# Performance work log

Measured on AMD Instinct MI355X. Metric: run time of the kernel, lower is better.

Reference implementation:

```python
import jax, jax.numpy as jnp
import numpy as np

DIM = 64          # RefineNet dim
MDIM = 32         # EGNN m_dim
NLAY = 16         # 4 refine stages x n_layer=4 EGNN layers
VOCAB = 26        # len(RNAAlphabet)
PAD = 1           # padding_idx
NPOS = 4096 + PAD + 1
N = 23            # atoms per residue (hard-coded repeat(1,1,23))
EIN = 2 * DIM + 1 # edge MLP input dim

silu = jax.nn.silu

def _lin(x, w, b):
    return x @ w + b

def _egnn(feats, coors, p):
    ew1, eb1, ew2, eb2, cw1, cb1, cw2, cb2, nw1, nb1, nw2, nb2, g, beta = p
    B, Nn, D = feats.shape
    rel = coors[:, :, None, :] - coors[:, None, :, :]            # [B,Nn,Nn,3]
    dist = jnp.sum(rel * rel, -1, keepdims=True)                 # [B,Nn,Nn,1]
    fi = jnp.broadcast_to(feats[:, :, None, :], (B, Nn, Nn, D))
    fj = jnp.broadcast_to(feats[:, None, :, :], (B, Nn, Nn, D))
    edge_in = jnp.concatenate([fi, fj, dist], -1)                # [B,Nn,Nn,2D+1]
    m_ij = silu(_lin(silu(_lin(edge_in, ew1, eb1)), ew2, eb2))   # [B,Nn,Nn,MDIM]
    w = _lin(silu(_lin(m_ij, cw1, cb1)), cw2, cb2)[..., 0]       # [B,Nn,Nn]
    nrm = jnp.sqrt(dist)
    normed = rel / jnp.maximum(nrm, 1e-8)
    # CoorsNorm uses LayerNorm over a size-1 dim: (x - mean) == 0, so phase == beta
    phase = g * jnp.zeros_like(nrm) + beta
    coors_out = jnp.einsum('bij,bijc->bic', w * (1.0 / 50.0), phase * normed) + coors
    m_i = m_ij.sum(-2)
    node_out = _lin(silu(_lin(jnp.concatenate([feats, m_i], -1), nw1, nb1)), nw2, nb2) + feats
    return node_out, coors_out

def _forward(tokens, cords, tok_emb, pos_emb, ew1, eb1, ew2, eb2,
             cw1, cb1, cw2, cb2, nw1, nb1, nw2, nb2, ln_g, ln_b):
    stacked = (ew1, eb1, ew2, eb2, cw1, cb1, cw2, cb2, nw1, nb1, nw2, nb2, ln_g, ln_b)
    t = tokens[:, 0, :]                                  # [b,l]
    b, l = t.shape
    tok = jnp.broadcast_to(t[:, :, None], (b, l, N))     # repeat(1,1,23)
    fea = tok_emb[tok]                                   # [b,l,N,DIM]
    mask = (tok.reshape(b * l, N) != PAD).astype(jnp.int32)
    pos = jnp.cumsum(mask, axis=1) * mask + PAD
    fea = fea + pos_emb[pos].reshape(fea.shape)
    co = cords.reshape(b, l, N, 3)

    def run(f, c, start):
        for k in range(4):
            p = tuple(a[start + k] for a in stacked)
            f, c = _egnn(f, c, p)
        return f, c

    f, c = run(fea.reshape(b * l, N, DIM), co.reshape(b * l, N, 3), 0)
    f = jnp.swapaxes(f.reshape(b, l, N, DIM), 1, 2)
    c = jnp.swapaxes(c.reshape(b, l, N, 3), 1, 2)
    f, c = run(f.reshape(b * N, l, DIM), c.reshape(b * N, l, 3), 4)
    f = jnp.swapaxes(f.reshape(b, N, l, DIM), 1, 2)
    c = jnp.swapaxes(c.reshape(b, N, l, 3), 1, 2)
    f, c = run(f.reshape(b * l, N, DIM), c.reshape(b * l, N, 3), 8)
    f = jnp.swapaxes(f.reshape(b, l, N, DIM), 1, 2)
    c = jnp.swapaxes(c.reshape(b, l, N, 3), 1, 2)
    f, c = run(f.reshape(b * N, l, DIM), c.reshape(b * N, l, 3), 12)
    c = jnp.swapaxes(c.reshape(b, N, l, 3), 1, 2)
    return c.reshape(b, l * N, 3)

def setup_inputs():
    key = jax.random.key(0)
    ks = jax.random.split(key, 20)
    b, l = 2, 96
    s = 0.02
    def W(k, shp):
        return jax.random.normal(k, shp, jnp.float32) * s
    return {
        "tokens": jax.random.randint(ks[0], (b, 1, l), 0, VOCAB),
        "cords": jax.random.normal(ks[1], (b, l * N, 3), jnp.float32),
        "tok_emb": W(ks[2], (VOCAB, DIM)),
        "pos_emb": W(ks[3], (NPOS, DIM)).at[PAD].set(0.0),
        "ew1": W(ks[4], (NLAY, EIN, EIN * 2)), "eb1": W(ks[5], (NLAY, EIN * 2)),
        "ew2": W(ks[6], (NLAY, EIN * 2, MDIM)), "eb2": W(ks[7], (NLAY, MDIM)),
        "cw1": W(ks[8], (NLAY, MDIM, MDIM * 4)), "cb1": W(ks[9], (NLAY, MDIM * 4)),
        "cw2": W(ks[10], (NLAY, MDIM * 4, 1)), "cb2": W(ks[11], (NLAY, 1)),
        "nw1": W(ks[12], (NLAY, DIM + MDIM, DIM * 2)), "nb1": W(ks[13], (NLAY, DIM * 2)),
        "nw2": W(ks[14], (NLAY, DIM * 2, DIM)), "nb2": W(ks[15], (NLAY, DIM)),
        "ln_g": 1.0 + W(ks[16], (NLAY, 1)),
        "ln_b": W(ks[17], (NLAY, 1)),
    }

def reference(tokens, cords, tok_emb, pos_emb, ew1, eb1, ew2, eb2,
              cw1, cb1, cw2, cb2, nw1, nb1, nw2, nb2, ln_g, ln_b):
    return _forward(tokens, cords, tok_emb, pos_emb, ew1, eb1, ew2, eb2,
                    cw1, cb1, cw2, cb2, nw1, nb1, nw2, nb2, ln_g, ln_b)
```

## Files before the change

### kernel.cpp

```cpp
#include <hip/hip_runtime.h>
#include <math.h>

#define DIM   64
#define MDIM  32
#define NLAY  16
#define PAD   1
#define NB    2
#define LL    96
#define NN    23
#define NNODE (NB*LL*NN)
#define EIN   129
#define EH    258
#define KP    272
#define NK0   17
#define NH    128
#define BPITCH 276
#define APITCH 276
#define NOUT  516
#define NTILE 17
#define XP    104
#define HP    136
#define OP    560

typedef __attribute__((ext_vector_type(8)))  short        bf16x8;
typedef __attribute__((ext_vector_type(16))) float        f32x16;
typedef __attribute__((ext_vector_type(4)))  unsigned int uint4v;
typedef __attribute__((ext_vector_type(2)))  float        f32x2;
typedef __attribute__((ext_vector_type(4)))  float        f32x4;

__device__ __forceinline__ f32x2 mk2(float a, float b) { f32x2 r; r.x = a; r.y = b; return r; }

__device__ __forceinline__ float silu_f(float x) {
    float e = __expf(-x);
    return x * __builtin_amdgcn_rcpf(1.0f + e);
}
__device__ __forceinline__ f32x2 silu2(f32x2 x) {
    f32x2 t = x * (-1.44269504f);
    f32x2 e;
    e.x = __builtin_amdgcn_exp2f(t.x);
    e.y = __builtin_amdgcn_exp2f(t.y);
    f32x2 den = e + 1.0f;
    f32x2 r;
    r.x = __builtin_amdgcn_rcpf(den.x);
    r.y = __builtin_amdgcn_rcpf(den.y);
    return x * r;
}
__device__ __forceinline__ unsigned short bf16_rn(float x) {
    unsigned u = __float_as_uint(x);
    u += 0x7FFF + ((u >> 16) & 1);
    return (unsigned short)(u >> 16);
}
__device__ __forceinline__ float bf16_up(unsigned short h) {
    return __uint_as_float(((unsigned)h) << 16);
}
__device__ __forceinline__ f32x2 ub2(unsigned bw) {
    return mk2(__uint_as_float(bw << 16), __uint_as_float(bw & 0xFFFF0000u));
}
__device__ __forceinline__ unsigned hpack(f32x2 a2, f32x2 w2, f32x2 b2, f32x2 d2) {
    f32x2 x2 = a2 + b2;
    x2 = __builtin_elementwise_fma(d2, w2, x2);
    f32x2 h2 = silu2(x2);
    return __builtin_amdgcn_perm(__float_as_uint(h2.y), __float_as_uint(h2.x), 0x07060302u);
}
__device__ __forceinline__ int fwd_map(int nf, int alongL) {
    if (alongL) {
        int b = nf / (LL * NN);
        int rem = nf % (LL * NN);
        int l = rem / NN, n = rem % NN;
        return (b * NN + n) * LL + l;
    }
    return nf;
}
__device__ __forceinline__ int inv_map(int gnode, int alongL) {
    if (alongL) {
        int g = gnode / LL, l = gnode % LL;
        int b = g / NN, n = g % NN;
        return (b * LL + l) * NN + n;
    }
    return gnode;
}

__global__ void k_embed(const int* __restrict__ tokens,
                        const float* __restrict__ tok_emb,
                        const float* __restrict__ pos_emb,
                        float* __restrict__ feats) {
    int idx = blockIdx.x * blockDim.x + threadIdx.x;
    if (idx < NNODE * DIM) {
        int node = idx / DIM, d = idx % DIM;
        int b = node / (LL * NN);
        int rem = node % (LL * NN);
        int n = rem % NN;
        int l = rem / NN;
        int t = tokens[b * LL + l];
        float f = tok_emb[t * DIM + d];
        if (t != PAD) f += pos_emb[(n + 2) * DIM + d];
        feats[idx] = f;
    }
}

__global__ void k_prep(const float* __restrict__ ew1, const float* __restrict__ ew2,
                       const float* __restrict__ cw1, const float* __restrict__ cb1,
                       const float* __restrict__ cw2,
                       const float* __restrict__ nw1, const float* __restrict__ nw2,
                       float* __restrict__ wdF, unsigned short* __restrict__ ew2P,
                       unsigned short* __restrict__ cw1P,
                       float* __restrict__ cbwP,
                       unsigned short* __restrict__ ew1P,
                       unsigned short* __restrict__ nw1P,
                       unsigned short* __restrict__ nw2P) {
    int idx = blockIdx.x * blockDim.x + threadIdx.x;
    if (idx < NLAY * KP) {
        int L = idx / KP, k = idx % KP;
        float v = (k < EH) ? ew1[(size_t)L * EIN * EH + 128 * EH + k] : 0.0f;
        wdF[idx] = bf16_up(bf16_rn(v));
    }
    if (idx < NLAY * NK0 * 512) {
        int L = idx / (NK0 * 512); int r = idx % (NK0 * 512);
        int k0 = r / 512; int r2 = r % 512;
        int lane = r2 >> 3, j = r2 & 7;
        int k = k0 * 16 + (lane >> 5) * 8 + j;
        int n = lane & 31;
        float v = (k < EH) ? ew2[((size_t)L * EH + k) * MDIM + n] : 0.0f;
        ew2P[idx] = bf16_rn(v);
    }
    if (idx < NLAY * 4096) {
        int L = idx / 4096; int r = idx % 4096;
        int mb = r / 1024; int r2 = r % 1024;
        int k0 = r2 / 512; int r3 = r2 % 512;
        int lane = r3 >> 3, j = r3 & 7;
        int k = k0 * 16 + (lane >> 5) * 8 + j;
        int o = mb * 32 + (lane & 31);
        cw1P[idx] = bf16_rn(cw1[((size_t)L * MDIM + k) * NH + o]);
    }
    if (idx < NLAY * 128) {
        int L = idx / 128; int r = idx % 128;
        int hlf = r / 64; int r2 = r % 64;
        int mb = r2 / 16, reg = r2 % 16;
        int o = mb * 32 + (reg & 3) + 8 * (reg >> 2) + 4 * hlf;
        cbwP[(size_t)L * 256 + r * 2 + 0] = cb1[L * NH + o];
        cbwP[(size_t)L * 256 + r * 2 + 1] = cw2[L * NH + o];
    }
    if (idx < NLAY * NTILE * 4 * 512) {
        int L = idx / (NTILE * 4 * 512); int r = idx % (NTILE * 4 * 512);
        int nt = r / 2048; int r2 = r % 2048;
        int ks = r2 / 512; int r3 = r2 % 512;
        int lane = r3 >> 3, j = r3 & 7;
        int d = ks * 16 + (lane >> 5) * 8 + j;
        int o = nt * 32 + (lane & 31);
        float v = 0.0f;
        if (o < EH)        v = ew1[(size_t)L * EIN * EH + d * EH + o];
        else if (o < NOUT) v = ew1[(size_t)L * EIN * EH + (DIM + d) * EH + (o - EH)];
        ew1P[idx] = bf16_rn(v);
    }
    if (idx < NLAY * 4 * 6 * 512) {
        int L = idx / 12288; int r = idx % 12288;
        int nt = r / 3072; int r2 = r % 3072;
        int ks = r2 / 512; int r3 = r2 % 512;
        int lane = r3 >> 3, j = r3 & 7;
        int k = ks * 16 + (lane >> 5) * 8 + j;
        int n = nt * 32 + (lane & 31);
        nw1P[idx] = bf16_rn(nw1[((size_t)L * (DIM + MDIM) + k) * NH + n]);
    }
    if (idx < NLAY * 2 * 8 * 512) {
        int L = idx / 8192; int r = idx % 8192;
        int nt = r / 4096; int r2 = r % 4096;
        int ks = r2 / 512; int r3 = r2 % 512;
        int lane = r3 >> 3, j = r3 & 7;
        int k = ks * 16 + (lane >> 5) * 8 + j;
        int n = nt * 32 + (lane & 31);
        nw2P[idx] = bf16_rn(nw2[((size_t)L * NH + k) * DIM + n]);
    }
}

__global__ __launch_bounds__(256)
void k_np(const float* __restrict__ fIn, const float* __restrict__ coSrc,
          const float* __restrict__ miL, const float* __restrict__ dL,
          const unsigned short* __restrict__ nw1PL, const float* __restrict__ nb1L,
          const unsigned short* __restrict__ nw2PL, const float* __restrict__ nb2L,
          const unsigned short* __restrict__ ew1PL, const float* __restrict__ eb1L,
          float* __restrict__ fOut, float* __restrict__ coDst,
          float* __restrict__ miNext, float* __restrict__ dNext,
          unsigned short* __restrict__ aH, unsigned short* __restrict__ bH,
          int aL0, int aL1, int doNode) {
    __shared__ unsigned short xS[32 * XP];
    __shared__ unsigned short hS[32 * HP];
    __shared__ unsigned short outS[32 * OP];
    __shared__ int gsrcS[32], gdstS[32];

    int n0  = blockIdx.x * 32;
    int tid = threadIdx.x;
    int wave = tid >> 6, lane = tid & 63, half = lane >> 5, e = lane & 31;

    if (tid < 32) {
        gsrcS[tid] = fwd_map(n0 + tid, aL0);
        gdstS[tid] = fwd_map(n0 + tid, aL1);
    }
    __syncthreads();

    for (int i = 0; i < 8; i++) {
        int x = tid + 256 * i;
        int node = x >> 6, d = x & 63;
        xS[node * XP + d] = bf16_rn(fIn[(n0 + node) * DIM + d]);
    }
    if (doNode) {
        for (int i = 0; i < 4; i++) {
            int x = tid + 256 * i;
            int node = x >> 5, d = x & 31;
            xS[node * XP + DIM + d] = bf16_rn(miL[(size_t)gsrcS[node] * MDIM + d]);
        }
    }
    for (int x = tid; x < 32 * 14; x += 256) {
        int node = x / 14, c = EH + x % 14;
        outS[node * OP + c] = 0;
    }
    if (tid < 96) {
        int node = tid / 3, c = tid % 3;
        int gs = gsrcS[node], gd = gdstS[node];
        float cv = coSrc[gs * 3 + c] + (doNode ? dL[gs * 3 + c] : 0.0f);
        coDst[gd * 3 + c] = cv;
        dNext[gd * 3 + c] = 0.0f;
    }
    for (int i = 0; i < 4; i++) {
        int x = tid + 256 * i;
        int node = x >> 5, d = x & 31;
        miNext[(size_t)gdstS[node] * MDIM + d] = 0.0f;
    }
    __syncthreads();

    if (doNode) {
        {
            int nt = wave;
            f32x16 acc;
#pragma unroll
            for (int q = 0; q < 16; q++) acc[q] = 0.0f;
#pragma unroll
            for (int ks = 0; ks < 6; ks++) {
                uint4v au = *(const uint4v*)(xS + e * XP + ks * 16 + half * 8);
                uint4v bu = *(const uint4v*)(nw1PL + ((size_t)(nt * 6 + ks) * 512 + lane * 8));
                acc = __builtin_amdgcn_mfma_f32_32x32x16_bf16(
                          __builtin_bit_cast(bf16x8, au),
                          __builtin_bit_cast(bf16x8, bu), acc, 0, 0, 0);
            }
            int o = nt * 32 + e;
            float b1 = nb1L[o];
#pragma unroll
            for (int q = 0; q < 16; q++) {
                int row = (q & 3) + 8 * (q >> 2) + 4 * half;
                hS[row * HP + o] = bf16_rn(silu_f(acc[q] + b1));
            }
        }
        __syncthreads();

        if (wave < 2) {
            int nt = wave;
            f32x16 acc;
#pragma unroll
            for (int q = 0; q < 16; q++) acc[q] = 0.0f;
#pragma unroll
            for (int ks = 0; ks < 8; ks++) {
                uint4v au = *(const uint4v*)(hS + e * HP + ks * 16 + half * 8);
                uint4v bu = *(const uint4v*)(nw2PL + ((size_t)(nt * 8 + ks) * 512 + lane * 8));
                acc = __builtin_amdgcn_mfma_f32_32x32x16_bf16(
                          __builtin_bit_cast(bf16x8, au),
                          __builtin_bit_cast(bf16x8, bu), acc, 0, 0, 0);
            }
            int o = nt * 32 + e;
            float b2 = nb2L[o];
#pragma unroll
            for (int q = 0; q < 16; q++) {
                int row = (q & 3) + 8 * (q >> 2) + 4 * half;
                float fo = acc[q] + b2 + bf16_up(xS[row * XP + o]);
                fOut[(size_t)(n0 + row) * DIM + o] = fo;
                xS[row * XP + o] = bf16_rn(fo);
            }
        }
        __syncthreads();
    }

    {
        uint4v afrag[4];
#pragma unroll
        for (int ks = 0; ks < 4; ks++)
            afrag[ks] = *(const uint4v*)(xS + e * XP + ks * 16 + half * 8);

        for (int nt = wave; nt < NTILE; nt += 4) {
            f32x16 acc;
#pragma unroll
            for (int q = 0; q < 16; q++) acc[q] = 0.0f;
#pragma unroll
            for (int ks = 0; ks < 4; ks++) {
                uint4v bu = *(const uint4v*)(ew1PL + ((size_t)(nt * 4 + ks) * 512 + lane * 8));
                acc = __builtin_amdgcn_mfma_f32_32x32x16_bf16(
                          __builtin_bit_cast(bf16x8, afrag[ks]),
                          __builtin_bit_cast(bf16x8, bu), acc, 0, 0, 0);
            }
            int o = nt * 32 + e;
            float eb = (o < EH) ? eb1L[o] : 0.0f;
            int col = (o < EH) ? o : (o + 14);
#pragma unroll
            for (int q = 0; q < 16; q++) {
                int row = (q & 3) + 8 * (q >> 2) + 4 * half;
                float v = (o < NOUT) ? (acc[q] + eb) : 0.0f;
                outS[row * OP + col] = bf16_rn(v);
            }
        }
    }
    __syncthreads();

    for (int x = tid; x < 32 * 68; x += 256) {
        int row = x / 68, off = x % 68;
        int gd = gdstS[row];
        uint4v v = *(const uint4v*)(outS + row * OP + off * 8);
        if (off < 34) *(uint4v*)(aH + (size_t)gd * KP + off * 8) = v;
        else          *(uint4v*)(bH + (size_t)gd * KP + (off - 34) * 8) = v;
    }
}

__global__ __launch_bounds__(256, 3)
void k_edge(const unsigned short* __restrict__ aH,
            const unsigned short* __restrict__ bH,
            const float* __restrict__ coorsO,
            const float* __restrict__ wdFL,
            const unsigned short* __restrict__ ew2PL,
            const float* __restrict__ eb2L,
            const unsigned short* __restrict__ cw1PL,
            const float* __restrict__ cbwPL,
            const float* __restrict__ cb2L,
            const float* __restrict__ lnbL,
            float* __restrict__ miBuf, float* __restrict__ deltaBuf,
            int Nn, int itpg, int njt) {
    __shared__ unsigned short bS[32 * BPITCH];
    __shared__ __align__(16) float aSf[8 * APITCH];
    __shared__ __align__(16) float wdS[KP];
    __shared__ float cjS[32 * 3];
    __shared__ __align__(16) float cbwS[256];
    __shared__ unsigned short mT[4][32 * 36];

    int bid = blockIdx.x;
    int g   = bid / (itpg * njt);
    int r   = bid % (itpg * njt);
    int it  = r / njt;
    int jt  = r % njt;

    int tid  = threadIdx.x;
    int wave = tid >> 6, lane = tid & 63, half = lane >> 5, e = lane & 31;

    int j0  = jt * 32;
    int njr = Nn - j0; if (njr > 32) njr = 32;
    int i0  = it * 8;
    int nir = Nn - i0; if (nir > 8) nir = 8;

    {
        const unsigned int* src = (const unsigned int*)(bH + (size_t)(g * Nn + j0) * KP);
        unsigned int* dst = (unsigned int*)bS;
        int tot = njr * 136;
        for (int x = tid; x < tot; x += 256) {
            int rr = x / 136, c = x % 136;
            dst[rr * (BPITCH / 2) + c] = src[rr * 136 + c];
        }
        const unsigned short* asrc = aH + (size_t)(g * Nn + i0) * KP;
        int at = nir * KP;
        for (int x = tid; x < at; x += 256) {
            int rr = x / KP, k = x % KP;
            aSf[rr * APITCH + k] = bf16_up(asrc[rr * KP + k]);
        }
        for (int x = tid; x < KP; x += 256) wdS[x] = wdFL[x];
        if (tid < njr * 3) cjS[tid] = coorsO[(g * Nn + j0) * 3 + tid];
        if (tid < 256) cbwS[tid] = cbwPL[tid];
    }
    __syncthreads();

    float eb2v = eb2L[e];
    float beta = lnbL[0];
    float cb2v = cb2L[0];

    int  jc     = (e < njr) ? e : (njr - 1);
    bool jvalid = (e < njr);
    float cjx = cjS[jc * 3 + 0], cjy = cjS[jc * 3 + 1], cjz = cjS[jc * 3 + 2];

    unsigned short* mW = &mT[wave][0];
    const unsigned short* bRow = bS + jc * BPITCH;

    int il0 = wave * 2, il1 = wave * 2 + 1;
    bool v0 = il0 < nir, v1 = il1 < nir;
    int gi0 = g * Nn + i0 + (v0 ? il0 : 0);
    int gi1 = g * Nn + i0 + (v1 ? il1 : 0);

    float rx0, ry0, rz0, d0, rx1, ry1, rz1, d1;
    {
        float cx = coorsO[gi0 * 3 + 0], cy = coorsO[gi0 * 3 + 1], cz = coorsO[gi0 * 3 + 2];
        rx0 = cx - cjx; ry0 = cy - cjy; rz0 = cz - cjz;
        d0 = rx0 * rx0 + ry0 * ry0 + rz0 * rz0;
        cx = coorsO[gi1 * 3 + 0]; cy = coorsO[gi1 * 3 + 1]; cz = coorsO[gi1 * 3 + 2];
        rx1 = cx - cjx; ry1 = cy - cjy; rz1 = cz - cjz;
        d1 = rx1 * rx1 + ry1 * ry1 + rz1 * rz1;
    }
    f32x2 d20 = mk2(d0, d0), d21 = mk2(d1, d1);
    const float* aR0 = aSf + (v0 ? il0 : 0) * APITCH;
    const float* aR1 = aSf + (v1 ? il1 : 0) * APITCH;

    f32x16 acc0, acc1;
#pragma unroll
    for (int q = 0; q < 16; q++) { acc0[q] = 0.0f; acc1[q] = 0.0f; }

#pragma unroll
    for (int k0 = 0; k0 < NK0; k0++) {
        int ko = k0 * 16 + half * 8;
        uint2 bA = *(const uint2*)(bRow + ko);
        uint2 bB = *(const uint2*)(bRow + ko + 4);
        f32x4 wv0 = *(const f32x4*)(wdS + ko);
        f32x4 wv1 = *(const f32x4*)(wdS + ko + 4);
        uint4v eu = *(const uint4v*)(ew2PL + ((size_t)k0 * 64 + lane) * 8);
        f32x2 b2_0 = ub2(bA.x), b2_1 = ub2(bA.y), b2_2 = ub2(bB.x), b2_3 = ub2(bB.y);

        f32x4 a00 = *(const f32x4*)(aR0 + ko);
        f32x4 a01 = *(const f32x4*)(aR0 + ko + 4);
        uint4v hu0;
        hu0[0] = hpack(a00.xy, wv0.xy, b2_0, d20);
        hu0[1] = hpack(a00.zw, wv0.zw, b2_1, d20);
        hu0[2] = hpack(a01.xy, wv1.xy, b2_2, d20);
        hu0[3] = hpack(a01.zw, wv1.zw, b2_3, d20);
        acc0 = __builtin_amdgcn_mfma_f32_32x32x16_bf16(
                   __builtin_bit_cast(bf16x8, hu0),
                   __builtin_bit_cast(bf16x8, eu), acc0, 0, 0, 0);

        f32x4 a10 = *(const f32x4*)(aR1 + ko);
        f32x4 a11 = *(const f32x4*)(aR1 + ko + 4);
        uint4v hu1;
        hu1[0] = hpack(a10.xy, wv0.xy, b2_0, d21);
        hu1[1] = hpack(a10.zw, wv0.zw, b2_1, d21);
        hu1[2] = hpack(a11.xy, wv1.xy, b2_2, d21);
        hu1[3] = hpack(a11.zw, wv1.zw, b2_3, d21);
        acc1 = __builtin_amdgcn_mfma_f32_32x32x16_bf16(
                   __builtin_bit_cast(bf16x8, hu1),
                   __builtin_bit_cast(bf16x8, eu), acc1, 0, 0, 0);
    }

    f32x2 ebp = mk2(eb2v, eb2v);

#pragma unroll
    for (int s = 0; s < 2; s++) {
        if (!(s ? v1 : v0)) continue;
        int gi = s ? gi1 : gi0;
        float rx = s ? rx1 : rx0, ry = s ? ry1 : ry0, rz = s ? rz1 : rz0;
        float dist = s ? d1 : d0;

        float mv[16];
        f32x2 mi2 = mk2(0.0f, 0.0f);
        if (njr == 32) {
#pragma unroll
            for (int qp = 0; qp < 8; qp++) {
                int q = qp * 2;
                f32x2 x2 = mk2(s ? acc1[q] : acc0[q], s ? acc1[q + 1] : acc0[q + 1]) + ebp;
                f32x2 m2 = silu2(x2);
                mv[q] = m2.x; mv[q + 1] = m2.y;
                mi2 += m2;
            }
        } else {
#pragma unroll
            for (int qp = 0; qp < 8; qp++) {
                int q = qp * 2;
                f32x2 x2 = mk2(s ? acc1[q] : acc0[q], s ? acc1[q + 1] : acc0[q + 1]) + ebp;
                f32x2 m2 = silu2(x2);
                int row0 = (q & 3) + 8 * (q >> 2) + 4 * half;
                if (j0 + row0 >= Nn) m2.x = 0.0f;
                if (j0 + row0 + 1 >= Nn) m2.y = 0.0f;
                mv[q] = m2.x; mv[q + 1] = m2.y;
                mi2 += m2;
            }
        }
        float miAcc = mi2.x + mi2.y;

#pragma unroll
        for (int q = 0; q < 4; q++) {
            unsigned lo = __builtin_amdgcn_perm(__float_as_uint(mv[q * 4 + 1]),
                                                __float_as_uint(mv[q * 4 + 0]), 0x07060302u);
            unsigned hi = __builtin_amdgcn_perm(__float_as_uint(mv[q * 4 + 3]),
                                                __float_as_uint(mv[q * 4 + 2]), 0x07060302u);
            int row0 = 8 * q + 4 * half;
            *(uint2*)&mW[e * 36 + row0] = make_uint2(lo, hi);
        }

        miAcc += __shfl_xor(miAcc, 32, 64);
        if (half == 0) atomicAdd(&miBuf[gi * MDIM + e], miAcc);

        bf16x8 bq[2];
#pragma unroll
        for (int k0 = 0; k0 < 2; k0++) {
            uint4v t;
#pragma unroll
            for (int p = 0; p < 4; p++) {
                unsigned w0 = mW[(k0 * 16 + half * 8 + 2 * p    ) * 36 + e];
                unsigned w1 = mW[(k0 * 16 + half * 8 + 2 * p + 1) * 36 + e];
                t[p] = w0 | (w1 << 16);
            }
            bq[k0] = __builtin_bit_cast(bf16x8, t);
        }

        f32x2 w2a = mk2(0.0f, 0.0f);
#pragma unroll
        for (int mb = 0; mb < 4; mb++) {
            f32x16 sacc;
#pragma unroll
            for (int q = 0; q < 16; q++) sacc[q] = 0.0f;
#pragma unroll
            for (int k0 = 0; k0 < 2; k0++) {
                uint4v cu = *(const uint4v*)(cw1PL + ((size_t)(mb * 2 + k0) * 64 + lane) * 8);
                sacc = __builtin_amdgcn_mfma_f32_32x32x16_bf16(
                           __builtin_bit_cast(bf16x8, cu), bq[k0], sacc, 0, 0, 0);
            }
            const f32x4* cv = (const f32x4*)(cbwS + (half * 4 + mb) * 32);
#pragma unroll
            for (int qp = 0; qp < 8; qp++) {
                f32x4 c4 = cv[qp];
                f32x2 s2 = mk2(sacc[2 * qp], sacc[2 * qp + 1]) + mk2(c4.x, c4.z);
                f32x2 p2 = silu2(s2);
                w2a = __builtin_elementwise_fma(p2, mk2(c4.y, c4.w), w2a);
            }
        }
        float wAcc = w2a.x + w2a.y;
        wAcc += __shfl_xor(wAcc, 32, 64);
        float w = wAcc + cb2v;
        float nrm = sqrtf(dist);
        float scale = (w * 0.02f) * beta * __builtin_amdgcn_rcpf(fmaxf(nrm, 1e-8f));

        float dAx = 0.0f, dAy = 0.0f, dAz = 0.0f;
        if (jvalid && half == 0) {
            dAx = scale * rx; dAy = scale * ry; dAz = scale * rz;
        }
#pragma unroll
        for (int m = 16; m >= 1; m >>= 1) {
            dAx += __shfl_xor(dAx, m, 64);
            dAy += __shfl_xor(dAy, m, 64);
            dAz += __shfl_xor(dAz, m, 64);
        }
        if (lane == 0) {
            atomicAdd(&deltaBuf[gi * 3 + 0], dAx);
            atomicAdd(&deltaBuf[gi * 3 + 1], dAy);
            atomicAdd(&deltaBuf[gi * 3 + 2], dAz);
        }
    }
}

__global__ void k_fin(const float* __restrict__ co, const float* __restrict__ dl,
                      float* __restrict__ out) {
    int idx = blockIdx.x * blockDim.x + threadIdx.x;
    if (idx < NNODE * 3) {
        int gnode = idx / 3, c = idx % 3;
        int nf = inv_map(gnode, 1);
        out[nf * 3 + c] = co[idx] + dl[idx];
    }
}

extern "C" void kernel_launch(void* const* d_in, const int* in_sizes, int n_in,
                              void* d_out, int out_size, void* d_ws, size_t ws_size,
                              hipStream_t stream) {
    (void)in_sizes; (void)n_in; (void)out_size; (void)ws_size;

    const int*   tokens  = (const int*)d_in[0];
    const float* cords   = (const float*)d_in[1];
    const float* tok_emb = (const float*)d_in[2];
    const float* pos_emb = (const float*)d_in[3];
    const float* ew1 = (const float*)d_in[4];
    const float* eb1 = (const float*)d_in[5];
    const float* ew2 = (const float*)d_in[6];
    const float* eb2 = (const float*)d_in[7];
    const float* cw1 = (const float*)d_in[8];
    const float* cb1 = (const float*)d_in[9];
    const float* cw2 = (const float*)d_in[10];
    const float* cb2 = (const float*)d_in[11];
    const float* nw1 = (const float*)d_in[12];
    const float* nb1 = (const float*)d_in[13];
    const float* nw2 = (const float*)d_in[14];
    const float* nb2 = (const float*)d_in[15];
    const float* lnb = (const float*)d_in[17];

    float* wf = (float*)d_ws;
    float* featsA = wf; wf += NNODE * DIM;
    float* featsB = wf; wf += NNODE * DIM;
    float* coorsO0 = wf; wf += NNODE * 3;
    float* coorsO1 = wf; wf += NNODE * 3;
    float* mi0  = wf; wf += NNODE * MDIM;
    float* mi1  = wf; wf += NNODE * MDIM;
    float* dl0  = wf; wf += NNODE * 3;
    float* dl1  = wf; wf += NNODE * 3;
    float* cbwP = wf; wf += NLAY * 256;
    float* wdF  = wf; wf += NLAY * KP;

    uintptr_t p = (uintptr_t)wf; p = (p + 15) & ~(uintptr_t)15;
    unsigned short* wh = (unsigned short*)p;
    unsigned short* aHb  = wh; wh += (size_t)NNODE * KP;
    unsigned short* bHb  = wh; wh += (size_t)NNODE * KP;
    unsigned short* ew2P = wh; wh += NLAY * NK0 * 512;
    unsigned short* cw1P = wh; wh += NLAY * 4096;
    unsigned short* ew1P = wh; wh += (size_t)NLAY * NTILE * 4 * 512;
    unsigned short* nw1P = wh; wh += (size_t)NLAY * 4 * 6 * 512;
    unsigned short* nw2P = wh; wh += (size_t)NLAY * 2 * 8 * 512;

    float* coorsO[2] = {coorsO0, coorsO1};
    float* miB[2]    = {mi0, mi1};
    float* dlB[2]    = {dl0, dl1};

    int prepN = NLAY * NTILE * 4 * 512;
    k_prep<<<(prepN + 255) / 256, 256, 0, stream>>>(
        ew1, ew2, cw1, cb1, cw2, nw1, nw2,
        wdF, ew2P, cw1P, cbwP, ew1P, nw1P, nw2P);
    k_embed<<<(NNODE * DIM + 255) / 256, 256, 0, stream>>>(
        tokens, tok_emb, pos_emb, featsA);

    float* fCur = featsA; float* fNxt = featsB;

    k_np<<<NNODE / 32, 256, 0, stream>>>(
        fCur, cords, nullptr, nullptr,
        nullptr, nullptr, nullptr, nullptr,
        ew1P + 0, eb1 + 0,
        fNxt, coorsO[0], miB[0], dlB[0],
        aHb, bHb, 0, 0, 0);

    for (int L = 0; L < NLAY; L++) {
        int alongL = (L / 4) % 2;
        int idx  = L & 1;
        int Nn   = alongL ? LL : NN;
        int njt  = alongL ? 3 : 1;
        int itpg = (Nn + 7) / 8;
        int groups = NNODE / Nn;

        k_edge<<<groups * itpg * njt, 256, 0, stream>>>(
            aHb, bHb, coorsO[idx],
            wdF + L * KP, ew2P + (size_t)L * NK0 * 512, eb2 + L * MDIM,
            cw1P + (size_t)L * 4096, cbwP + (size_t)L * 256,
            cb2 + L, lnb + L, miB[idx], dlB[idx], Nn, itpg, njt);

        if (L < NLAY - 1) {
            int aL1 = ((L + 1) / 4) % 2;
            int nidx = (L + 1) & 1;
            k_np<<<NNODE / 32, 256, 0, stream>>>(
                fCur, coorsO[idx], miB[idx], dlB[idx],
                nw1P + (size_t)L * 4 * 6 * 512, nb1 + L * NH,
                nw2P + (size_t)L * 2 * 8 * 512, nb2 + L * DIM,
                ew1P + (size_t)(L + 1) * NTILE * 4 * 512, eb1 + (size_t)(L + 1) * EH,
                fNxt, coorsO[nidx], miB[nidx], dlB[nidx],
                aHb, bHb, alongL, aL1, 1);
            float* t = fCur; fCur = fNxt; fNxt = t;
        } else {
            k_fin<<<(NNODE * 3 + 255) / 256, 256, 0, stream>>>(
                coorsO[idx], dlB[idx], (float*)d_out);
        }
    }
}
```

Before: 972.0 us.

## Split node-projection kernel across four blocks per tile and batch silu reciprocals

The node/projection kernel now launches four blocks per 32-node tile. Each block computes the node MLP redundantly but only a quarter of the edge-input projection column tiles, with column padding realigned to 18 tiles so each half maps cleanly onto the aH/bH buffers. Separately, silu is evaluated four lanes at a time, sharing one reciprocal across four denominators, in the edge hidden activation, message activation and coordinate-weight MLP. This trades redundant node-MLP work and extra blocks for more parallelism, and trades fewer rcp instructions for extra multiplies and some overflow risk in the product of denominators.

```diff
diff --git a/kernel.cpp b/kernel.cpp
--- a/kernel.cpp
+++ b/kernel.cpp
@@ -16,11 +16,10 @@
 #define NH    128
 #define BPITCH 276
 #define APITCH 276
-#define NOUT  516
-#define NTILE 17
+#define NT2   18
 #define XP    104
 #define HP    136
-#define OP    560
+#define OPS   168
 
 typedef __attribute__((ext_vector_type(8)))  short        bf16x8;
 typedef __attribute__((ext_vector_type(16))) float        f32x16;
@@ -29,21 +28,29 @@
 typedef __attribute__((ext_vector_type(4)))  float        f32x4;
 
 __device__ __forceinline__ f32x2 mk2(float a, float b) { f32x2 r; r.x = a; r.y = b; return r; }
+__device__ __forceinline__ f32x4 mk4(float a, float b, float c, float d) {
+    f32x4 r; r.x = a; r.y = b; r.z = c; r.w = d; return r;
+}
 
 __device__ __forceinline__ float silu_f(float x) {
     float e = __expf(-x);
     return x * __builtin_amdgcn_rcpf(1.0f + e);
 }
-__device__ __forceinline__ f32x2 silu2(f32x2 x) {
-    f32x2 t = x * (-1.44269504f);
-    f32x2 e;
+__device__ __forceinline__ f32x4 silu4(f32x4 x) {
+    f32x4 t = x * (-1.44269504f);
+    f32x4 e;
     e.x = __builtin_amdgcn_exp2f(t.x);
     e.y = __builtin_amdgcn_exp2f(t.y);
-    f32x2 den = e + 1.0f;
-    f32x2 r;
-    r.x = __builtin_amdgcn_rcpf(den.x);
-    r.y = __builtin_amdgcn_rcpf(den.y);
-    return x * r;
+    e.z = __builtin_amdgcn_exp2f(t.z);
+    e.w = __builtin_amdgcn_exp2f(t.w);
+    f32x4 d = e + 1.0f;
+    float p01 = d.x * d.y, p23 = d.z * d.w;
+    float R = __builtin_amdgcn_rcpf(p01 * p23);
+    float R01 = R * p23, R23 = R * p01;
+    f32x4 sg;
+    sg.x = d.y * R01; sg.y = d.x * R01;
+    sg.z = d.w * R23; sg.w = d.z * R23;
+    return x * sg;
 }
 __device__ __forceinline__ unsigned short bf16_rn(float x) {
     unsigned u = __float_as_uint(x);
@@ -53,14 +60,21 @@
 __device__ __forceinline__ float bf16_up(unsigned short h) {
     return __uint_as_float(((unsigned)h) << 16);
 }
-__device__ __forceinline__ f32x2 ub2(unsigned bw) {
-    return mk2(__uint_as_float(bw << 16), __uint_as_float(bw & 0xFFFF0000u));
-}
-__device__ __forceinline__ unsigned hpack(f32x2 a2, f32x2 w2, f32x2 b2, f32x2 d2) {
-    f32x2 x2 = a2 + b2;
-    x2 = __builtin_elementwise_fma(d2, w2, x2);
-    f32x2 h2 = silu2(x2);
-    return __builtin_amdgcn_perm(__float_as_uint(h2.y), __float_as_uint(h2.x), 0x07060302u);
+__device__ __forceinline__ uint2 hpack4(f32x4 a4, f32x4 w4, unsigned bu0, unsigned bu1,
+                                        float dist) {
+    f32x4 b4;
+    b4.x = __uint_as_float(bu0 << 16);
+    b4.y = __uint_as_float(bu0 & 0xFFFF0000u);
+    b4.z = __uint_as_float(bu1 << 16);
+    b4.w = __uint_as_float(bu1 & 0xFFFF0000u);
+    f32x4 x4 = a4 + b4;
+    f32x4 d4 = mk4(dist, dist, dist, dist);
+    x4 = __builtin_elementwise_fma(d4, w4, x4);
+    f32x4 h4 = silu4(x4);
+    uint2 o;
+    o.x = __builtin_amdgcn_perm(__float_as_uint(h4.y), __float_as_uint(h4.x), 0x07060302u);
+    o.y = __builtin_amdgcn_perm(__float_as_uint(h4.w), __float_as_uint(h4.z), 0x07060302u);
+    return o;
 }
 __device__ __forceinline__ int fwd_map(int nf, int alongL) {
     if (alongL) {
@@ -140,16 +154,16 @@
         cbwP[(size_t)L * 256 + r * 2 + 0] = cb1[L * NH + o];
         cbwP[(size_t)L * 256 + r * 2 + 1] = cw2[L * NH + o];
     }
-    if (idx < NLAY * NTILE * 4 * 512) {
-        int L = idx / (NTILE * 4 * 512); int r = idx % (NTILE * 4 * 512);
+    if (idx < NLAY * NT2 * 4 * 512) {
+        int L = idx / (NT2 * 4 * 512); int r = idx % (NT2 * 4 * 512);
         int nt = r / 2048; int r2 = r % 2048;
         int ks = r2 / 512; int r3 = r2 % 512;
         int lane = r3 >> 3, j = r3 & 7;
         int d = ks * 16 + (lane >> 5) * 8 + j;
-        int o = nt * 32 + (lane & 31);
+        int c = nt * 32 + (lane & 31);
         float v = 0.0f;
-        if (o < EH)        v = ew1[(size_t)L * EIN * EH + d * EH + o];
-        else if (o < NOUT) v = ew1[(size_t)L * EIN * EH + (DIM + d) * EH + (o - EH)];
+        if (c < 288) { if (c < EH) v = ew1[(size_t)L * EIN * EH + d * EH + c]; }
+        else { int ob = c - 288; if (ob < EH) v = ew1[(size_t)L * EIN * EH + (DIM + d) * EH + ob]; }
         ew1P[idx] = bf16_rn(v);
     }
     if (idx < NLAY * 4 * 6 * 512) {
@@ -184,10 +198,12 @@
           int aL0, int aL1, int doNode) {
     __shared__ unsigned short xS[32 * XP];
     __shared__ unsigned short hS[32 * HP];
-    __shared__ unsigned short outS[32 * OP];
+    __shared__ unsigned short outS[32 * OPS];
     __shared__ int gsrcS[32], gdstS[32];
 
-    int n0  = blockIdx.x * 32;
+    int bid  = blockIdx.x;
+    int tileB = bid >> 2, par = bid & 3;
+    int n0  = tileB * 32;
     int tid = threadIdx.x;
     int wave = tid >> 6, lane = tid & 63, half = lane >> 5, e = lane & 31;
 
@@ -209,21 +225,19 @@
             xS[node * XP + DIM + d] = bf16_rn(miL[(size_t)gsrcS[node] * MDIM + d]);
         }
     }
-    for (int x = tid; x < 32 * 14; x += 256) {
-        int node = x / 14, c = EH + x % 14;
-        outS[node * OP + c] = 0;
-    }
-    if (tid < 96) {
-        int node = tid / 3, c = tid % 3;
-        int gs = gsrcS[node], gd = gdstS[node];
-        float cv = coSrc[gs * 3 + c] + (doNode ? dL[gs * 3 + c] : 0.0f);
-        coDst[gd * 3 + c] = cv;
-        dNext[gd * 3 + c] = 0.0f;
-    }
-    for (int i = 0; i < 4; i++) {
-        int x = tid + 256 * i;
-        int node = x >> 5, d = x & 31;
-        miNext[(size_t)gdstS[node] * MDIM + d] = 0.0f;
+    if (par == 0) {
+        if (tid < 96) {
+            int node = tid / 3, c = tid % 3;
+            int gs = gsrcS[node], gd = gdstS[node];
+            float cv = coSrc[gs * 3 + c] + (doNode ? dL[gs * 3 + c] : 0.0f);
+            coDst[gd * 3 + c] = cv;
+            dNext[gd * 3 + c] = 0.0f;
+        }
+        for (int i = 0; i < 4; i++) {
+            int x = tid + 256 * i;
+            int node = x >> 5, d = x & 31;
+            miNext[(size_t)gdstS[node] * MDIM + d] = 0.0f;
+        }
     }
     __syncthreads();
 
@@ -270,7 +284,7 @@
             for (int q = 0; q < 16; q++) {
                 int row = (q & 3) + 8 * (q >> 2) + 4 * half;
                 float fo = acc[q] + b2 + bf16_up(xS[row * XP + o]);
-                fOut[(size_t)(n0 + row) * DIM + o] = fo;
+                if (par == 0) fOut[(size_t)(n0 + row) * DIM + o] = fo;
                 xS[row * XP + o] = bf16_rn(fo);
             }
         }
@@ -283,7 +297,9 @@
         for (int ks = 0; ks < 4; ks++)
             afrag[ks] = *(const uint4v*)(xS + e * XP + ks * 16 + half * 8);
 
-        for (int nt = wave; nt < NTILE; nt += 4) {
+        for (int lt = wave; lt < 5; lt += 4) {
+            int nt = par + lt * 4;
+            if (nt >= NT2) continue;
             f32x16 acc;
 #pragma unroll
             for (int q = 0; q < 16; q++) acc[q] = 0.0f;
@@ -294,25 +310,37 @@
                           __builtin_bit_cast(bf16x8, afrag[ks]),
                           __builtin_bit_cast(bf16x8, bu), acc, 0, 0, 0);
             }
-            int o = nt * 32 + e;
-            float eb = (o < EH) ? eb1L[o] : 0.0f;
-            int col = (o < EH) ? o : (o + 14);
+            int c = nt * 32 + e;
+            bool isA = c < 288;
+            int oc = isA ? c : (c - 288);
+            bool valid = oc < EH;
+            float eb = (isA && valid) ? eb1L[oc] : 0.0f;
 #pragma unroll
             for (int q = 0; q < 16; q++) {
                 int row = (q & 3) + 8 * (q >> 2) + 4 * half;
-                float v = (o < NOUT) ? (acc[q] + eb) : 0.0f;
-                outS[row * OP + col] = bf16_rn(v);
+                float v = valid ? (acc[q] + eb) : 0.0f;
+                outS[row * OPS + lt * 32 + e] = bf16_rn(v);
             }
         }
     }
     __syncthreads();
 
-    for (int x = tid; x < 32 * 68; x += 256) {
-        int row = x / 68, off = x % 68;
-        int gd = gdstS[row];
-        uint4v v = *(const uint4v*)(outS + row * OP + off * 8);
-        if (off < 34) *(uint4v*)(aH + (size_t)gd * KP + off * 8) = v;
-        else          *(uint4v*)(bH + (size_t)gd * KP + (off - 34) * 8) = v;
+    {
+        int nch = (par < 2) ? 20 : 16;
+        for (int x = tid; x < 32 * nch; x += 256) {
+            int row = x / nch, cl = x % nch;
+            int lt = cl >> 2, sub = cl & 3;
+            int nt = par + lt * 4;
+            uint4v v = *(const uint4v*)(outS + row * OPS + lt * 32 + sub * 8);
+            int gd = gdstS[row];
+            if (nt < 9) {
+                int col = nt * 32 + sub * 8;
+                if (col < KP) *(uint4v*)(aH + (size_t)gd * KP + col) = v;
+            } else {
+                int col = (nt - 9) * 32 + sub * 8;
+                if (col < KP) *(uint4v*)(bH + (size_t)gd * KP + col) = v;
+            }
+        }
     }
 }
 
@@ -395,7 +423,6 @@
         rx1 = cx - cjx; ry1 = cy - cjy; rz1 = cz - cjz;
         d1 = rx1 * rx1 + ry1 * ry1 + rz1 * rz1;
     }
-    f32x2 d20 = mk2(d0, d0), d21 = mk2(d1, d1);
     const float* aR0 = aSf + (v0 ? il0 : 0) * APITCH;
     const float* aR1 = aSf + (v1 ? il1 : 0) * APITCH;
 
@@ -411,32 +438,27 @@
         f32x4 wv0 = *(const f32x4*)(wdS + ko);
         f32x4 wv1 = *(const f32x4*)(wdS + ko + 4);
         uint4v eu = *(const uint4v*)(ew2PL + ((size_t)k0 * 64 + lane) * 8);
-        f32x2 b2_0 = ub2(bA.x), b2_1 = ub2(bA.y), b2_2 = ub2(bB.x), b2_3 = ub2(bB.y);
 
         f32x4 a00 = *(const f32x4*)(aR0 + ko);
         f32x4 a01 = *(const f32x4*)(aR0 + ko + 4);
+        uint2 h00 = hpack4(a00, wv0, bA.x, bA.y, d0);
+        uint2 h01 = hpack4(a01, wv1, bB.x, bB.y, d0);
         uint4v hu0;
-        hu0[0] = hpack(a00.xy, wv0.xy, b2_0, d20);
-        hu0[1] = hpack(a00.zw, wv0.zw, b2_1, d20);
-        hu0[2] = hpack(a01.xy, wv1.xy, b2_2, d20);
-        hu0[3] = hpack(a01.zw, wv1.zw, b2_3, d20);
+        hu0[0] = h00.x; hu0[1] = h00.y; hu0[2] = h01.x; hu0[3] = h01.y;
         acc0 = __builtin_amdgcn_mfma_f32_32x32x16_bf16(
                    __builtin_bit_cast(bf16x8, hu0),
                    __builtin_bit_cast(bf16x8, eu), acc0, 0, 0, 0);
 
         f32x4 a10 = *(const f32x4*)(aR1 + ko);
         f32x4 a11 = *(const f32x4*)(aR1 + ko + 4);
+        uint2 h10 = hpack4(a10, wv0, bA.x, bA.y, d1);
+        uint2 h11 = hpack4(a11, wv1, bB.x, bB.y, d1);
         uint4v hu1;
-        hu1[0] = hpack(a10.xy, wv0.xy, b2_0, d21);
-        hu1[1] = hpack(a10.zw, wv0.zw, b2_1, d21);
-        hu1[2] = hpack(a11.xy, wv1.xy, b2_2, d21);
-        hu1[3] = hpack(a11.zw, wv1.zw, b2_3, d21);
+        hu1[0] = h10.x; hu1[1] = h10.y; hu1[2] = h11.x; hu1[3] = h11.y;
         acc1 = __builtin_amdgcn_mfma_f32_32x32x16_bf16(
                    __builtin_bit_cast(bf16x8, hu1),
                    __builtin_bit_cast(bf16x8, eu), acc1, 0, 0, 0);
     }
-
-    f32x2 ebp = mk2(eb2v, eb2v);
 
 #pragma unroll
     for (int s = 0; s < 2; s++) {
@@ -446,30 +468,25 @@
         float dist = s ? d1 : d0;
 
         float mv[16];
-        f32x2 mi2 = mk2(0.0f, 0.0f);
-        if (njr == 32) {
-#pragma unroll
-            for (int qp = 0; qp < 8; qp++) {
-                int q = qp * 2;
-                f32x2 x2 = mk2(s ? acc1[q] : acc0[q], s ? acc1[q + 1] : acc0[q + 1]) + ebp;
-                f32x2 m2 = silu2(x2);
-                mv[q] = m2.x; mv[q + 1] = m2.y;
-                mi2 += m2;
-            }
-        } else {
-#pragma unroll
-            for (int qp = 0; qp < 8; qp++) {
-                int q = qp * 2;
-                f32x2 x2 = mk2(s ? acc1[q] : acc0[q], s ? acc1[q + 1] : acc0[q + 1]) + ebp;
-                f32x2 m2 = silu2(x2);
-                int row0 = (q & 3) + 8 * (q >> 2) + 4 * half;
-                if (j0 + row0 >= Nn) m2.x = 0.0f;
-                if (j0 + row0 + 1 >= Nn) m2.y = 0.0f;
-                mv[q] = m2.x; mv[q + 1] = m2.y;
-                mi2 += m2;
-            }
-        }
-        float miAcc = mi2.x + mi2.y;
+        f32x4 mi4 = mk4(0.0f, 0.0f, 0.0f, 0.0f);
+#pragma unroll
+        for (int qg = 0; qg < 4; qg++) {
+            int q = qg * 4;
+            f32x4 x4 = mk4(s ? acc1[q] : acc0[q], s ? acc1[q + 1] : acc0[q + 1],
+                           s ? acc1[q + 2] : acc0[q + 2], s ? acc1[q + 3] : acc0[q + 3])
+                       + eb2v;
+            f32x4 m4 = silu4(x4);
+            if (njr != 32) {
+                int row0 = 8 * qg + 4 * half;
+                if (j0 + row0 + 0 >= Nn) m4.x = 0.0f;
+                if (j0 + row0 + 1 >= Nn) m4.y = 0.0f;
+                if (j0 + row0 + 2 >= Nn) m4.z = 0.0f;
+                if (j0 + row0 + 3 >= Nn) m4.w = 0.0f;
+            }
+            mv[q] = m4.x; mv[q + 1] = m4.y; mv[q + 2] = m4.z; mv[q + 3] = m4.w;
+            mi4 += m4;
+        }
+        float miAcc = (mi4.x + mi4.y) + (mi4.z + mi4.w);
 
 #pragma unroll
         for (int q = 0; q < 4; q++) {
@@ -497,7 +514,7 @@
             bq[k0] = __builtin_bit_cast(bf16x8, t);
         }
 
-        f32x2 w2a = mk2(0.0f, 0.0f);
+        f32x4 w4a = mk4(0.0f, 0.0f, 0.0f, 0.0f);
 #pragma unroll
         for (int mb = 0; mb < 4; mb++) {
             f32x16 sacc;
@@ -511,14 +528,15 @@
             }
             const f32x4* cv = (const f32x4*)(cbwS + (half * 4 + mb) * 32);
 #pragma unroll
-            for (int qp = 0; qp < 8; qp++) {
-                f32x4 c4 = cv[qp];
-                f32x2 s2 = mk2(sacc[2 * qp], sacc[2 * qp + 1]) + mk2(c4.x, c4.z);
-                f32x2 p2 = silu2(s2);
-                w2a = __builtin_elementwise_fma(p2, mk2(c4.y, c4.w), w2a);
-            }
-        }
-        float wAcc = w2a.x + w2a.y;
+            for (int i = 0; i < 4; i++) {
+                f32x4 c0 = cv[2 * i], c1 = cv[2 * i + 1];
+                f32x4 x4 = mk4(sacc[4 * i] + c0.x, sacc[4 * i + 1] + c0.z,
+                               sacc[4 * i + 2] + c1.x, sacc[4 * i + 3] + c1.z);
+                f32x4 p4 = silu4(x4);
+                w4a = __builtin_elementwise_fma(p4, mk4(c0.y, c0.w, c1.y, c1.w), w4a);
+            }
+        }
+        float wAcc = (w4a.x + w4a.y) + (w4a.z + w4a.w);
         wAcc += __shfl_xor(wAcc, 32, 64);
         float w = wAcc + cb2v;
         float nrm = sqrtf(dist);
@@ -593,7 +611,7 @@
     unsigned short* bHb  = wh; wh += (size_t)NNODE * KP;
     unsigned short* ew2P = wh; wh += NLAY * NK0 * 512;
     unsigned short* cw1P = wh; wh += NLAY * 4096;
-    unsigned short* ew1P = wh; wh += (size_t)NLAY * NTILE * 4 * 512;
+    unsigned short* ew1P = wh; wh += (size_t)NLAY * NT2 * 4 * 512;
     unsigned short* nw1P = wh; wh += (size_t)NLAY * 4 * 6 * 512;
     unsigned short* nw2P = wh; wh += (size_t)NLAY * 2 * 8 * 512;
 
@@ -601,7 +619,7 @@
     float* miB[2]    = {mi0, mi1};
     float* dlB[2]    = {dl0, dl1};
 
-    int prepN = NLAY * NTILE * 4 * 512;
+    int prepN = NLAY * NT2 * 4 * 512;
     k_prep<<<(prepN + 255) / 256, 256, 0, stream>>>(
         ew1, ew2, cw1, cb1, cw2, nw1, nw2,
         wdF, ew2P, cw1P, cbwP, ew1P, nw1P, nw2P);
@@ -610,7 +628,7 @@
 
     float* fCur = featsA; float* fNxt = featsB;
 
-    k_np<<<NNODE / 32, 256, 0, stream>>>(
+    k_np<<<(NNODE / 32) * 4, 256, 0, stream>>>(
         fCur, cords, nullptr, nullptr,
         nullptr, nullptr, nullptr, nullptr,
         ew1P + 0, eb1 + 0,
@@ -634,11 +652,11 @@
         if (L < NLAY - 1) {
             int aL1 = ((L + 1) / 4) % 2;
             int nidx = (L + 1) & 1;
-            k_np<<<NNODE / 32, 256, 0, stream>>>(
+            k_np<<<(NNODE / 32) * 4, 256, 0, stream>>>(
                 fCur, coorsO[idx], miB[idx], dlB[idx],
                 nw1P + (size_t)L * 4 * 6 * 512, nb1 + L * NH,
                 nw2P + (size_t)L * 2 * 8 * 512, nb2 + L * DIM,
-                ew1P + (size_t)(L + 1) * NTILE * 4 * 512, eb1 + (size_t)(L + 1) * EH,
+                ew1P + (size_t)(L + 1) * NT2 * 4 * 512, eb1 + (size_t)(L + 1) * EH,
                 fNxt, coorsO[nidx], miB[nidx], dlB[nidx],
                 aHb, bHb, alongL, aL1, 1);
             float* t = fCur; fCur = fNxt; fNxt = t;
```

Result: no change. 962.4 us (-1.0%).

## Split node-projection kernel across four blocks per node tile

Applied to the files above, without the earlier changes.

The k_np kernel now launches four blocks per 32-node tile. Each block recomputes the node MLP redundantly and then produces only a quarter of the edge-projection output tiles, using a column layout repacked to 18 tiles so the A and B halves are padded separately. The goal is more parallelism and better GPU occupancy in a kernel that previously ran few blocks, each doing serial MFMA tile loops. The cost is four times the node-MLP compute and the feature and weight loads, with only block 0 writing the shared outputs.

```diff
diff --git a/kernel.cpp b/kernel.cpp
--- a/kernel.cpp
+++ b/kernel.cpp
@@ -16,11 +16,10 @@
 #define NH    128
 #define BPITCH 276
 #define APITCH 276
-#define NOUT  516
-#define NTILE 17
+#define NT2   18
 #define XP    104
 #define HP    136
-#define OP    560
+#define OPS   168
 
 typedef __attribute__((ext_vector_type(8)))  short        bf16x8;
 typedef __attribute__((ext_vector_type(16))) float        f32x16;
@@ -140,16 +139,16 @@
         cbwP[(size_t)L * 256 + r * 2 + 0] = cb1[L * NH + o];
         cbwP[(size_t)L * 256 + r * 2 + 1] = cw2[L * NH + o];
     }
-    if (idx < NLAY * NTILE * 4 * 512) {
-        int L = idx / (NTILE * 4 * 512); int r = idx % (NTILE * 4 * 512);
+    if (idx < NLAY * NT2 * 4 * 512) {
+        int L = idx / (NT2 * 4 * 512); int r = idx % (NT2 * 4 * 512);
         int nt = r / 2048; int r2 = r % 2048;
         int ks = r2 / 512; int r3 = r2 % 512;
         int lane = r3 >> 3, j = r3 & 7;
         int d = ks * 16 + (lane >> 5) * 8 + j;
-        int o = nt * 32 + (lane & 31);
+        int c = nt * 32 + (lane & 31);
         float v = 0.0f;
-        if (o < EH)        v = ew1[(size_t)L * EIN * EH + d * EH + o];
-        else if (o < NOUT) v = ew1[(size_t)L * EIN * EH + (DIM + d) * EH + (o - EH)];
+        if (c < 288) { if (c < EH) v = ew1[(size_t)L * EIN * EH + d * EH + c]; }
+        else { int ob = c - 288; if (ob < EH) v = ew1[(size_t)L * EIN * EH + (DIM + d) * EH + ob]; }
         ew1P[idx] = bf16_rn(v);
     }
     if (idx < NLAY * 4 * 6 * 512) {
@@ -184,10 +183,12 @@
           int aL0, int aL1, int doNode) {
     __shared__ unsigned short xS[32 * XP];
     __shared__ unsigned short hS[32 * HP];
-    __shared__ unsigned short outS[32 * OP];
+    __shared__ unsigned short outS[32 * OPS];
     __shared__ int gsrcS[32], gdstS[32];
 
-    int n0  = blockIdx.x * 32;
+    int bid  = blockIdx.x;
+    int tileB = bid >> 2, par = bid & 3;
+    int n0  = tileB * 32;
     int tid = threadIdx.x;
     int wave = tid >> 6, lane = tid & 63, half = lane >> 5, e = lane & 31;
 
@@ -209,21 +210,19 @@
             xS[node * XP + DIM + d] = bf16_rn(miL[(size_t)gsrcS[node] * MDIM + d]);
         }
     }
-    for (int x = tid; x < 32 * 14; x += 256) {
-        int node = x / 14, c = EH + x % 14;
-        outS[node * OP + c] = 0;
-    }
-    if (tid < 96) {
-        int node = tid / 3, c = tid % 3;
-        int gs = gsrcS[node], gd = gdstS[node];
-        float cv = coSrc[gs * 3 + c] + (doNode ? dL[gs * 3 + c] : 0.0f);
-        coDst[gd * 3 + c] = cv;
-        dNext[gd * 3 + c] = 0.0f;
-    }
-    for (int i = 0; i < 4; i++) {
-        int x = tid + 256 * i;
-        int node = x >> 5, d = x & 31;
-        miNext[(size_t)gdstS[node] * MDIM + d] = 0.0f;
+    if (par == 0) {
+        if (tid < 96) {
+            int node = tid / 3, c = tid % 3;
+            int gs = gsrcS[node], gd = gdstS[node];
+            float cv = coSrc[gs * 3 + c] + (doNode ? dL[gs * 3 + c] : 0.0f);
+            coDst[gd * 3 + c] = cv;
+            dNext[gd * 3 + c] = 0.0f;
+        }
+        for (int i = 0; i < 4; i++) {
+            int x = tid + 256 * i;
+            int node = x >> 5, d = x & 31;
+            miNext[(size_t)gdstS[node] * MDIM + d] = 0.0f;
+        }
     }
     __syncthreads();
 
@@ -270,7 +269,7 @@
             for (int q = 0; q < 16; q++) {
                 int row = (q & 3) + 8 * (q >> 2) + 4 * half;
                 float fo = acc[q] + b2 + bf16_up(xS[row * XP + o]);
-                fOut[(size_t)(n0 + row) * DIM + o] = fo;
+                if (par == 0) fOut[(size_t)(n0 + row) * DIM + o] = fo;
                 xS[row * XP + o] = bf16_rn(fo);
             }
         }
@@ -283,7 +282,9 @@
         for (int ks = 0; ks < 4; ks++)
             afrag[ks] = *(const uint4v*)(xS + e * XP + ks * 16 + half * 8);
 
-        for (int nt = wave; nt < NTILE; nt += 4) {
+        for (int lt = wave; lt < 5; lt += 4) {
+            int nt = par + lt * 4;
+            if (nt >= NT2) continue;
             f32x16 acc;
 #pragma unroll
             for (int q = 0; q < 16; q++) acc[q] = 0.0f;
@@ -294,25 +295,37 @@
                           __builtin_bit_cast(bf16x8, afrag[ks]),
                           __builtin_bit_cast(bf16x8, bu), acc, 0, 0, 0);
             }
-            int o = nt * 32 + e;
-            float eb = (o < EH) ? eb1L[o] : 0.0f;
-            int col = (o < EH) ? o : (o + 14);
+            int c = nt * 32 + e;
+            bool isA = c < 288;
+            int oc = isA ? c : (c - 288);
+            bool valid = oc < EH;
+            float eb = (isA && valid) ? eb1L[oc] : 0.0f;
 #pragma unroll
             for (int q = 0; q < 16; q++) {
                 int row = (q & 3) + 8 * (q >> 2) + 4 * half;
-                float v = (o < NOUT) ? (acc[q] + eb) : 0.0f;
-                outS[row * OP + col] = bf16_rn(v);
+                float v = valid ? (acc[q] + eb) : 0.0f;
+                outS[row * OPS + lt * 32 + e] = bf16_rn(v);
             }
         }
     }
     __syncthreads();
 
-    for (int x = tid; x < 32 * 68; x += 256) {
-        int row = x / 68, off = x % 68;
-        int gd = gdstS[row];
-        uint4v v = *(const uint4v*)(outS + row * OP + off * 8);
-        if (off < 34) *(uint4v*)(aH + (size_t)gd * KP + off * 8) = v;
-        else          *(uint4v*)(bH + (size_t)gd * KP + (off - 34) * 8) = v;
+    {
+        int nch = (par < 2) ? 20 : 16;
+        for (int x = tid; x < 32 * nch; x += 256) {
+            int row = x / nch, cl = x % nch;
+            int lt = cl >> 2, sub = cl & 3;
+            int nt = par + lt * 4;
+            uint4v v = *(const uint4v*)(outS + row * OPS + lt * 32 + sub * 8);
+            int gd = gdstS[row];
+            if (nt < 9) {
+                int col = nt * 32 + sub * 8;
+                if (col < KP) *(uint4v*)(aH + (size_t)gd * KP + col) = v;
+            } else {
+                int col = (nt - 9) * 32 + sub * 8;
+                if (col < KP) *(uint4v*)(bH + (size_t)gd * KP + col) = v;
+            }
+        }
     }
 }
 
@@ -593,7 +606,7 @@
     unsigned short* bHb  = wh; wh += (size_t)NNODE * KP;
     unsigned short* ew2P = wh; wh += NLAY * NK0 * 512;
     unsigned short* cw1P = wh; wh += NLAY * 4096;
-    unsigned short* ew1P = wh; wh += (size_t)NLAY * NTILE * 4 * 512;
+    unsigned short* ew1P = wh; wh += (size_t)NLAY * NT2 * 4 * 512;
     unsigned short* nw1P = wh; wh += (size_t)NLAY * 4 * 6 * 512;
     unsigned short* nw2P = wh; wh += (size_t)NLAY * 2 * 8 * 512;
 
@@ -601,7 +614,7 @@
     float* miB[2]    = {mi0, mi1};
     float* dlB[2]    = {dl0, dl1};
 
-    int prepN = NLAY * NTILE * 4 * 512;
+    int prepN = NLAY * NT2 * 4 * 512;
     k_prep<<<(prepN + 255) / 256, 256, 0, stream>>>(
         ew1, ew2, cw1, cb1, cw2, nw1, nw2,
         wdF, ew2P, cw1P, cbwP, ew1P, nw1P, nw2P);
@@ -610,7 +623,7 @@
 
     float* fCur = featsA; float* fNxt = featsB;
 
-    k_np<<<NNODE / 32, 256, 0, stream>>>(
+    k_np<<<(NNODE / 32) * 4, 256, 0, stream>>>(
         fCur, cords, nullptr, nullptr,
         nullptr, nullptr, nullptr, nullptr,
         ew1P + 0, eb1 + 0,
@@ -634,11 +647,11 @@
         if (L < NLAY - 1) {
             int aL1 = ((L + 1) / 4) % 2;
             int nidx = (L + 1) & 1;
-            k_np<<<NNODE / 32, 256, 0, stream>>>(
+            k_np<<<(NNODE / 32) * 4, 256, 0, stream>>>(
                 fCur, coorsO[idx], miB[idx], dlB[idx],
                 nw1P + (size_t)L * 4 * 6 * 512, nb1 + L * NH,
                 nw2P + (size_t)L * 2 * 8 * 512, nb2 + L * DIM,
-                ew1P + (size_t)(L + 1) * NTILE * 4 * 512, eb1 + (size_t)(L + 1) * EH,
+                ew1P + (size_t)(L + 1) * NT2 * 4 * 512, eb1 + (size_t)(L + 1) * EH,
                 fNxt, coorsO[nidx], miB[nidx], dlB[nidx],
                 aHb, bHb, alongL, aL1, 1);
             float* t = fCur; fCur = fNxt; fNxt = t;
```

Result: faster. 932.1 us (-4.1%).
